# Optimization experiments

Hardware: AMD Instinct MI355X
Metric: run time of the kernel (lower is better)

Reference implementation:

```python
import jax, jax.numpy as jnp
import numpy as np

B, T, D = 2, 2048, 2048
H, KVH, HD = 32, 8, 64
N_REP = H // KVH


def setup_inputs() -> dict:
    key = jax.random.key(0)
    ks = jax.random.split(key, 7)
    x = jax.random.normal(ks[0], (B, T, D), dtype=jnp.float32)
    # rope tables: [max_seq, head_dim//2]
    cos = jax.random.uniform(ks[1], (T, HD // 2), dtype=jnp.float32, minval=-1.0, maxval=1.0)
    sin = jax.random.uniform(ks[2], (T, HD // 2), dtype=jnp.float32, minval=-1.0, maxval=1.0)
    s = 0.02
    wq = jax.random.normal(ks[3], (D, H * HD), dtype=jnp.float32) * s
    wk = jax.random.normal(ks[4], (D, KVH * HD), dtype=jnp.float32) * s
    wv = jax.random.normal(ks[5], (D, KVH * HD), dtype=jnp.float32) * s
    wo = jax.random.normal(ks[6], (H * HD, D), dtype=jnp.float32) * s
    return {"x": x, "cos": cos, "sin": sin, "wq": wq, "wk": wk, "wv": wv, "wo": wo}


def _rotate(t):
    h = t.shape[-1] // 2
    return jnp.concatenate([-t[..., h:], t[..., :h]], axis=-1)


def reference(x, cos, sin, wq, wk, wv, wo):
    b, t, _ = x.shape
    # projections -> [B, heads, T, HD]
    q = (x @ wq).reshape(b, t, H, HD).transpose(0, 2, 1, 3)
    k = (x @ wk).reshape(b, t, KVH, HD).transpose(0, 2, 1, 3)
    v = (x @ wv).reshape(b, t, KVH, HD).transpose(0, 2, 1, 3)
    # rope: cos/sin tiled (concat) to full head_dim, broadcast over batch/head
    cos_f = jnp.tile(cos[:t], (1, 2))[None, None]  # [1,1,T,HD]
    sin_f = jnp.tile(sin[:t], (1, 2))[None, None]
    q = q * cos_f + _rotate(q) * sin_f
    k = k * cos_f + _rotate(k) * sin_f
    # GQA: repeat kv heads
    k = jnp.repeat(k, N_REP, axis=1)
    v = jnp.repeat(v, N_REP, axis=1)
    scale = 1.0 / np.sqrt(HD).astype(np.float32)
    scores = jnp.einsum('bhqd,bhkd->bhqk', q, k) * scale
    causal = jnp.tril(jnp.ones((t, t), dtype=bool))
    scores = jnp.where(causal, scores, jnp.float32(-1e30))
    attn = jax.nn.softmax(scores, axis=-1)
    out = jnp.einsum('bhqk,bhkd->bhqd', attn, v)
    out = out.transpose(0, 2, 1, 3).reshape(b, t, H * HD)
    return out @ wo
```

## Files before the change

kernel.cpp:

```cpp
#include <hip/hip_runtime.h>
#include <hip/hip_bf16.h>
#include <cstdint>

typedef unsigned short u16;
typedef unsigned int u32;
typedef __bf16 bf16x8 __attribute__((ext_vector_type(8)));
typedef float f32x4 __attribute__((ext_vector_type(4)));
typedef float f32x16 __attribute__((ext_vector_type(16)));

#define BATCH 2
#define SEQ 2048
#define DMODEL 2048
#define NH 32
#define NKVH 8
#define HD 64
#define NQROWS (BATCH*SEQ)
#define QCOLS (NH*HD)
#define KVCOLS (NKVH*HD)
#define NCAT (QCOLS+2*KVCOLS)

static __device__ __forceinline__ u16 f2bf(float f) {
  u32 u = __float_as_uint(f);
  return (u16)((u + 0x7fffu + ((u >> 16) & 1u)) >> 16);
}

#define GLOAD16(gp, lp) __builtin_amdgcn_global_load_lds( \
    (const __attribute__((address_space(1))) void*)(gp),  \
    (__attribute__((address_space(3))) void*)(lp), 16, 0, 0)

__global__ __launch_bounds__(256) void k_cvt_bf16(const float* __restrict__ in,
                                                  u16* __restrict__ out, int n4) {
  int i = blockIdx.x * 256 + threadIdx.x;
  if (i >= n4) return;
  float4 v = reinterpret_cast<const float4*>(in)[i];
  ushort4 o;
  o.x = f2bf(v.x); o.y = f2bf(v.y); o.z = f2bf(v.z); o.w = f2bf(v.w);
  reinterpret_cast<ushort4*>(out)[i] = o;
}

__global__ __launch_bounds__(256) void k_transpose_all(const float* __restrict__ wq,
                                                       const float* __restrict__ wk,
                                                       const float* __restrict__ wv,
                                                       const float* __restrict__ wo,
                                                       u16* __restrict__ wcatT,
                                                       u16* __restrict__ woT) {
  __shared__ float tile[32][33];
  const int tidx = blockIdx.x;
  const float* src; u16* dst; int C, c0, r0;
  if (tidx < 4096) {
    src = wq; dst = wcatT; C = QCOLS;
    c0 = (tidx & 63) * 32; r0 = (tidx >> 6) * 32;
  } else if (tidx < 5120) {
    int t2 = tidx - 4096;
    src = wk; dst = wcatT + (size_t)QCOLS * DMODEL; C = KVCOLS;
    c0 = (t2 & 15) * 32; r0 = (t2 >> 4) * 32;
  } else if (tidx < 6144) {
    int t2 = tidx - 5120;
    src = wv; dst = wcatT + (size_t)(QCOLS + KVCOLS) * DMODEL; C = KVCOLS;
    c0 = (t2 & 15) * 32; r0 = (t2 >> 4) * 32;
  } else {
    int t2 = tidx - 6144;
    src = wo; dst = woT; C = DMODEL;
    c0 = (t2 & 63) * 32; r0 = (t2 >> 6) * 32;
  }
  const int R = 2048;
  int tx = threadIdx.x & 31, ty = threadIdx.x >> 5;
#pragma unroll
  for (int i = 0; i < 4; i++)
    tile[ty * 4 + i][tx] = src[(size_t)(r0 + ty * 4 + i) * C + c0 + tx];
  __syncthreads();
#pragma unroll
  for (int i = 0; i < 4; i++)
    dst[(size_t)(c0 + ty * 4 + i) * R + r0 + tx] = f2bf(tile[tx][ty * 4 + i]);
}

template<int EPI>
__global__ __launch_bounds__(256) void k_gemm(const u16* __restrict__ A,
                                              const u16* __restrict__ BT,
                                              void* __restrict__ Cout,
                                              int M, int N, int K,
                                              const float* __restrict__ cosb,
                                              const float* __restrict__ sinb,
                                              u16* __restrict__ dstK,
                                              u16* __restrict__ dstV) {
  __shared__ __align__(16) u16 As[2][128 * 32];
  __shared__ __align__(16) u16 Bs[2][128 * 32];
  const int tid = threadIdx.x;
  const int w = tid >> 6, l = tid & 63;
  const int l15 = l & 15, l4 = l >> 4;

  const int nwg = gridDim.x * gridDim.y;
  int hwid = blockIdx.y * gridDim.x + blockIdx.x;
  int wk = (hwid & 7) * (nwg >> 3) + (hwid >> 3);
  const int bx = wk % gridDim.x, by = wk / gridDim.x;

  const int m0 = by * 128, n0 = bx * 128;
  const int wr = w >> 1, wc = w & 1;

  const u16* ga = A + (size_t)(m0 + w * 32 + (l >> 2)) * K + (l & 3) * 8;
  const u16* gb = BT + (size_t)(n0 + w * 32 + (l >> 2)) * K + (l & 3) * 8;
  const int af_off = (wr * 64 + l15) * 32 + l4 * 8;
  const int bf_off = (wc * 64 + l15) * 32 + l4 * 8;

  auto stage = [&](int buf, int kt) {
    const u16* ga_ = ga + kt;
    const u16* gb_ = gb + kt;
    u16* asb = &As[buf][w * 1024];
    u16* bsb = &Bs[buf][w * 1024];
    GLOAD16(ga_, asb);
    GLOAD16(ga_ + 16 * (size_t)K, asb + 512);
    GLOAD16(gb_, bsb);
    GLOAD16(gb_ + 16 * (size_t)K, bsb + 512);
  };

  f32x4 acc[4][4] = {};
  stage(0, 0);
  __syncthreads();

  int cur = 0;
  for (int kt = 0; kt < K; kt += 32) {
    if (kt + 32 < K) stage(cur ^ 1, kt + 32);
    bf16x8 af[4], bfv[4];
#pragma unroll
    for (int mi = 0; mi < 4; mi++)
      af[mi] = *reinterpret_cast<const bf16x8*>(&As[cur][af_off + mi * 512]);
#pragma unroll
    for (int ni = 0; ni < 4; ni++)
      bfv[ni] = *reinterpret_cast<const bf16x8*>(&Bs[cur][bf_off + ni * 512]);
#pragma unroll
    for (int mi = 0; mi < 4; mi++)
#pragma unroll
      for (int ni = 0; ni < 4; ni++)
        acc[mi][ni] = __builtin_amdgcn_mfma_f32_16x16x32_bf16(af[mi], bfv[ni], acc[mi][ni], 0, 0, 0);
    __syncthreads();
    cur ^= 1;
  }

  const int row0 = m0 + wr * 64 + l4 * 4;
  const int col0 = n0 + wc * 64 + l15;
  if constexpr (EPI == 1) {
    float* C = (float*)Cout;
#pragma unroll
    for (int mi = 0; mi < 4; mi++)
#pragma unroll
      for (int ni = 0; ni < 4; ni++)
#pragma unroll
        for (int j = 0; j < 4; j++)
          C[(size_t)(row0 + mi * 16 + j) * N + col0 + ni * 16] = acc[mi][ni][j];
  } else {
    if (n0 < QCOLS + KVCOLS) {
#pragma unroll
      for (int mi = 0; mi < 4; mi++)
#pragma unroll
        for (int j = 0; j < 4; j++) {
          int t = (row0 + mi * 16 + j) & (SEQ - 1);
#pragma unroll
          for (int ni = 0; ni < 2; ni++) {
            int d = ni * 16 + l15;
            float c = cosb[t * 32 + d], s = sinb[t * 32 + d];
            float a = acc[mi][ni][j], bb = acc[mi][ni + 2][j];
            acc[mi][ni][j]     = a * c - bb * s;
            acc[mi][ni + 2][j] = bb * c + a * s;
          }
        }
      if (n0 < QCOLS) {
        const float QSC = 0.125f * 1.44269504088896f;
        u16* C = (u16*)Cout;
#pragma unroll
        for (int mi = 0; mi < 4; mi++)
#pragma unroll
          for (int ni = 0; ni < 4; ni++)
#pragma unroll
            for (int j = 0; j < 4; j++)
              C[(size_t)(row0 + mi * 16 + j) * QCOLS + col0 + ni * 16] = f2bf(acc[mi][ni][j] * QSC);
      } else {
        int kc0 = col0 - QCOLS;
#pragma unroll
        for (int mi = 0; mi < 4; mi++)
#pragma unroll
          for (int ni = 0; ni < 4; ni++)
#pragma unroll
            for (int j = 0; j < 4; j++)
              dstK[(size_t)(row0 + mi * 16 + j) * KVCOLS + kc0 + ni * 16] = f2bf(acc[mi][ni][j]);
      }
    } else {
      int vc0 = col0 - (QCOLS + KVCOLS);
#pragma unroll
      for (int mi = 0; mi < 4; mi++) {
        int row = row0 + mi * 16;
        int b = row >> 11, t = row & (SEQ - 1);
#pragma unroll
        for (int ni = 0; ni < 4; ni++) {
          ushort4 v;
          v.x = f2bf(acc[mi][ni][0]);
          v.y = f2bf(acc[mi][ni][1]);
          v.z = f2bf(acc[mi][ni][2]);
          v.w = f2bf(acc[mi][ni][3]);
          *reinterpret_cast<ushort4*>(&dstV[((size_t)b * KVCOLS + vc0 + ni * 16) * SEQ + t]) = v;
        }
      }
    }
  }
}

__global__ __launch_bounds__(128, 3) void k_attn(const u16* __restrict__ Q,
                                                 const u16* __restrict__ K,
                                                 const u16* __restrict__ VT,
                                                 u16* __restrict__ AO) {
  __shared__ __align__(16) u16 Ks[2][4096];
  __shared__ __align__(16) u16 Vs[2][4096];
  const int tid = threadIdx.x;
  const int w = tid >> 6, l = tid & 63;
  const int lo = l & 31, hi = l >> 5;
  const int id = blockIdx.y * gridDim.x + blockIdx.x;
  const int bh = (id & 7) * 8 + ((id >> 3) & 7);
  const int bxx = id >> 6;
  const int b = bh >> 5, h = bh & 31, g = h >> 2;
  const int srow = l >> 3;
  const int scol = l & 7;

  const u16* Kbase = K + ((size_t)b * SEQ) * KVCOLS + g * 64;
  const u16* Vbase = VT + ((size_t)(b * KVCOLS + g * 64)) * SEQ;

  for (int half = 0; half < 2; half++) {
    const int qt = half ? (31 - bxx) : bxx;
    const int qbase = qt * 64 + w * 32;
    const int nkc = qt + 1;
    const int qloc = w * 32 + lo;

    bf16x8 qf[4];
    {
      const u16* qp = Q + (size_t)(b * SEQ + qbase + lo) * QCOLS + h * 64 + hi * 8;
#pragma unroll
      for (int kb = 0; kb < 4; kb++)
        qf[kb] = *reinterpret_cast<const bf16x8*>(qp + kb * 16);
    }
    f32x16 oacc[2] = {};
    float ls0 = 0.f, ls1 = 0.f;

#pragma unroll
    for (int i = 0; i < 4; i++) {
      int r = w * 32 + i * 8 + srow;
      int cs = scol ^ (srow & 7);
      GLOAD16(Kbase + (size_t)r * KVCOLS + cs * 8, &Ks[0][(w * 32 + i * 8) * 64 + l * 8]);
      GLOAD16(Vbase + (size_t)r * SEQ + cs * 8, &Vs[0][(w * 32 + i * 8) * 64 + l * 8]);
    }
    __syncthreads();

    for (int kc = 0; kc < nkc; kc++) {
      const int bi = kc & 1;
      if (kc + 1 < nkc) {
#pragma unroll
        for (int i = 0; i < 4; i++) {
          int r = w * 32 + i * 8 + srow;
          int cs = scol ^ (srow & 7);
          GLOAD16(Kbase + (size_t)((kc + 1) * 64 + r) * KVCOLS + cs * 8,
                  &Ks[bi ^ 1][(w * 32 + i * 8) * 64 + l * 8]);
          GLOAD16(Vbase + (size_t)r * SEQ + (kc + 1) * 64 + cs * 8,
                  &Vs[bi ^ 1][(w * 32 + i * 8) * 64 + l * 8]);
        }
      }
      f32x16 sacc[2] = {};
      __builtin_amdgcn_s_setprio(1);
#pragma unroll
      for (int t = 0; t < 2; t++) {
#pragma unroll
        for (int kb = 0; kb < 4; kb++) {
          int row = t * 32 + lo;
          int slot = (2 * kb + hi) ^ (lo & 7);
          bf16x8 kf = *reinterpret_cast<const bf16x8*>(&Ks[bi][row * 64 + slot * 8]);
          sacc[t] = __builtin_amdgcn_mfma_f32_32x32x16_bf16(kf, qf[kb], sacc[t], 0, 0, 0);
        }
      }
      __builtin_amdgcn_s_setprio(0);

      const bool diag = (kc == qt);
      u32 u[2][4][2];
#pragma unroll
      for (int t = 0; t < 2; t++) {
        float pv[16];
#pragma unroll
        for (int r = 0; r < 16; r++) {
          float e = exp2f(sacc[t][r]);
          if (diag) {
            int kvoff = t * 32 + (r & 3) + 8 * (r >> 2) + 4 * hi;
            if (kvoff > qloc) e = 0.f;
          }
          pv[r] = e;
          if (t == 0) ls0 += e; else ls1 += e;
        }
#pragma unroll
        for (int qd = 0; qd < 4; qd++)
#pragma unroll
          for (int hh = 0; hh < 2; hh++) {
            u32 uu;
            asm("v_cvt_pk_bf16_f32 %0, %1, %2"
                : "=v"(uu) : "v"(pv[qd * 4 + 2 * hh]), "v"(pv[qd * 4 + 2 * hh + 1]));
            u[t][qd][hh] = uu;
          }
      }

#pragma unroll
      for (int km = 0; km < 4; km++) {
        const int t = km >> 1, p = km & 1;
        u32 a0 = u[t][2 * p][0], b0 = u[t][2 * p + 1][0];
        u32 a1 = u[t][2 * p][1], b1 = u[t][2 * p + 1][1];
        asm("v_permlane32_swap_b32 %0, %1" : "+v"(a0), "+v"(b0));
        asm("v_permlane32_swap_b32 %0, %1" : "+v"(a1), "+v"(b1));
        union { u32 uu[4]; bf16x8 v; } pa;
        pa.uu[0] = a0; pa.uu[1] = a1; pa.uu[2] = b0; pa.uu[3] = b1;
        __builtin_amdgcn_s_setprio(1);
#pragma unroll
        for (int td = 0; td < 2; td++) {
          int row = td * 32 + lo;
          int slot = (2 * km + hi) ^ (lo & 7);
          bf16x8 vf = *reinterpret_cast<const bf16x8*>(&Vs[bi][row * 64 + slot * 8]);
          oacc[td] = __builtin_amdgcn_mfma_f32_32x32x16_bf16(pa.v, vf, oacc[td], 0, 0, 0);
        }
        __builtin_amdgcn_s_setprio(0);
      }
      __syncthreads();
    }
    float tot = ls0 + ls1;
    tot += __shfl_xor(tot, 32);
#pragma unroll
    for (int r = 0; r < 16; r++) {
      int qr = (r & 3) + 8 * (r >> 2) + 4 * hi;
      float den = __shfl(tot, qr);
      float rv = __builtin_amdgcn_rcpf(den);
      size_t rowbase = (size_t)(b * SEQ + qbase + qr) * QCOLS + h * 64 + lo;
      AO[rowbase]      = f2bf(oacc[0][r] * rv);
      AO[rowbase + 32] = f2bf(oacc[1][r] * rv);
    }
  }
}

extern "C" void kernel_launch(void* const* d_in, const int* in_sizes, int n_in,
                              void* d_out, int out_size, void* d_ws, size_t ws_size,
                              hipStream_t stream) {
  const float* x    = (const float*)d_in[0];
  const float* cosb = (const float*)d_in[1];
  const float* sinb = (const float*)d_in[2];
  const float* wq   = (const float*)d_in[3];
  const float* wk   = (const float*)d_in[4];
  const float* wv   = (const float*)d_in[5];
  const float* wo   = (const float*)d_in[6];
  float* out = (float*)d_out;

  char* ws = (char*)d_ws;
  size_t off = 0;
  auto alloc = [&](size_t bytes) -> void* {
    void* p = ws + off;
    off += (bytes + 255) & ~(size_t)255;
    return p;
  };
  u16* xb    = (u16*)alloc((size_t)NQROWS * DMODEL * 2);
  u16* wcatT = (u16*)alloc((size_t)NCAT * DMODEL * 2);
  u16* woT   = (u16*)alloc((size_t)DMODEL * QCOLS * 2);
  u16* Qb    = (u16*)alloc((size_t)NQROWS * QCOLS * 2);
  u16* Kb    = (u16*)alloc((size_t)NQROWS * KVCOLS * 2);
  u16* VTb   = (u16*)alloc((size_t)BATCH * KVCOLS * SEQ * 2);
  u16* AO    = (u16*)alloc((size_t)NQROWS * QCOLS * 2);

  k_cvt_bf16<<<dim3(NQROWS * DMODEL / 4 / 256), dim3(256), 0, stream>>>(x, xb, NQROWS * DMODEL / 4);
  k_transpose_all<<<dim3(10240), dim3(256), 0, stream>>>(wq, wk, wv, wo, wcatT, woT);

  k_gemm<3><<<dim3(NCAT / 128, NQROWS / 128), 256, 0, stream>>>(
      xb, wcatT, Qb, NQROWS, NCAT, DMODEL, cosb, sinb, Kb, VTb);

  k_attn<<<dim3(16, BATCH * NH), 128, 0, stream>>>(Qb, Kb, VTb, AO);

  k_gemm<1><<<dim3(DMODEL / 128, NQROWS / 128), 256, 0, stream>>>(
      AO, woT, out, NQROWS, DMODEL, QCOLS, nullptr, nullptr, nullptr, nullptr);
}
```

Measured before the change: 214.5 us.

## Use single-wave attention blocks with 32-row tiles and waitcnt-based pipelining

```diff
diff --git a/kernel.cpp b/kernel.cpp
--- a/kernel.cpp
+++ b/kernel.cpp
@@ -203,108 +203,99 @@
   }
 }
 
-__global__ __launch_bounds__(128, 3) void k_attn(const u16* __restrict__ Q,
-                                                 const u16* __restrict__ K,
-                                                 const u16* __restrict__ VT,
-                                                 u16* __restrict__ AO) {
-  __shared__ __align__(16) u16 Ks[2][4096];
-  __shared__ __align__(16) u16 Vs[2][4096];
-  const int tid = threadIdx.x;
-  const int w = tid >> 6, l = tid & 63;
+__global__ __launch_bounds__(64, 3) void k_attn(const u16* __restrict__ Q,
+                                                const u16* __restrict__ K,
+                                                const u16* __restrict__ VT,
+                                                u16* __restrict__ AO) {
+  __shared__ __align__(16) u16 Ks[2][2048];
+  __shared__ __align__(16) u16 Vs[2][2048];
+  const int l = threadIdx.x;
   const int lo = l & 31, hi = l >> 5;
   const int id = blockIdx.y * gridDim.x + blockIdx.x;
   const int bh = (id & 7) * 8 + ((id >> 3) & 7);
   const int bxx = id >> 6;
   const int b = bh >> 5, h = bh & 31, g = h >> 2;
-  const int srow = l >> 3;
-  const int scol = l & 7;
 
   const u16* Kbase = K + ((size_t)b * SEQ) * KVCOLS + g * 64;
   const u16* Vbase = VT + ((size_t)(b * KVCOLS + g * 64)) * SEQ;
 
+  const int ksrow = l >> 3, kscol = l & 7;
+  const int kcs = kscol ^ ksrow;
+  const int vsrow = l >> 2, vscol = l & 3;
+  const int vcs = vscol ^ (vsrow & 3);
+
+  auto stage = [&](int kc, int buf) {
+#pragma unroll
+    for (int i = 0; i < 4; i++) {
+      GLOAD16(Kbase + (size_t)(kc * 32 + i * 8 + ksrow) * KVCOLS + kcs * 8,
+              &Ks[buf][i * 512 + l * 8]);
+      GLOAD16(Vbase + (size_t)(i * 16 + vsrow) * SEQ + kc * 32 + vcs * 8,
+              &Vs[buf][i * 512 + l * 8]);
+    }
+  };
+
   for (int half = 0; half < 2; half++) {
-    const int qt = half ? (31 - bxx) : bxx;
-    const int qbase = qt * 64 + w * 32;
+    const int qt = half ? (63 - bxx) : bxx;
+    const int q0 = qt * 32;
     const int nkc = qt + 1;
-    const int qloc = w * 32 + lo;
 
     bf16x8 qf[4];
     {
-      const u16* qp = Q + (size_t)(b * SEQ + qbase + lo) * QCOLS + h * 64 + hi * 8;
+      const u16* qp = Q + (size_t)(b * SEQ + q0 + lo) * QCOLS + h * 64 + hi * 8;
 #pragma unroll
       for (int kb = 0; kb < 4; kb++)
         qf[kb] = *reinterpret_cast<const bf16x8*>(qp + kb * 16);
     }
     f32x16 oacc[2] = {};
-    float ls0 = 0.f, ls1 = 0.f;
-
-#pragma unroll
-    for (int i = 0; i < 4; i++) {
-      int r = w * 32 + i * 8 + srow;
-      int cs = scol ^ (srow & 7);
-      GLOAD16(Kbase + (size_t)r * KVCOLS + cs * 8, &Ks[0][(w * 32 + i * 8) * 64 + l * 8]);
-      GLOAD16(Vbase + (size_t)r * SEQ + cs * 8, &Vs[0][(w * 32 + i * 8) * 64 + l * 8]);
-    }
-    __syncthreads();
-
+    float ls = 0.f;
+
+    stage(0, 0);
+    int bi = 0;
     for (int kc = 0; kc < nkc; kc++) {
-      const int bi = kc & 1;
       if (kc + 1 < nkc) {
-#pragma unroll
-        for (int i = 0; i < 4; i++) {
-          int r = w * 32 + i * 8 + srow;
-          int cs = scol ^ (srow & 7);
-          GLOAD16(Kbase + (size_t)((kc + 1) * 64 + r) * KVCOLS + cs * 8,
-                  &Ks[bi ^ 1][(w * 32 + i * 8) * 64 + l * 8]);
-          GLOAD16(Vbase + (size_t)r * SEQ + (kc + 1) * 64 + cs * 8,
-                  &Vs[bi ^ 1][(w * 32 + i * 8) * 64 + l * 8]);
-        }
-      }
-      f32x16 sacc[2] = {};
+        stage(kc + 1, bi ^ 1);
+        asm volatile("s_waitcnt vmcnt(8)" ::: "memory");
+      } else {
+        asm volatile("s_waitcnt vmcnt(0)" ::: "memory");
+      }
+      __builtin_amdgcn_sched_barrier(0);
+
+      f32x16 sacc = {};
       __builtin_amdgcn_s_setprio(1);
 #pragma unroll
-      for (int t = 0; t < 2; t++) {
-#pragma unroll
-        for (int kb = 0; kb < 4; kb++) {
-          int row = t * 32 + lo;
-          int slot = (2 * kb + hi) ^ (lo & 7);
-          bf16x8 kf = *reinterpret_cast<const bf16x8*>(&Ks[bi][row * 64 + slot * 8]);
-          sacc[t] = __builtin_amdgcn_mfma_f32_32x32x16_bf16(kf, qf[kb], sacc[t], 0, 0, 0);
-        }
+      for (int kb = 0; kb < 4; kb++) {
+        int slot = (2 * kb + hi) ^ (lo & 7);
+        bf16x8 kf = *reinterpret_cast<const bf16x8*>(&Ks[bi][lo * 64 + slot * 8]);
+        sacc = __builtin_amdgcn_mfma_f32_32x32x16_bf16(kf, qf[kb], sacc, 0, 0, 0);
       }
       __builtin_amdgcn_s_setprio(0);
 
       const bool diag = (kc == qt);
-      u32 u[2][4][2];
-#pragma unroll
-      for (int t = 0; t < 2; t++) {
-        float pv[16];
-#pragma unroll
-        for (int r = 0; r < 16; r++) {
-          float e = exp2f(sacc[t][r]);
-          if (diag) {
-            int kvoff = t * 32 + (r & 3) + 8 * (r >> 2) + 4 * hi;
-            if (kvoff > qloc) e = 0.f;
-          }
-          pv[r] = e;
-          if (t == 0) ls0 += e; else ls1 += e;
-        }
-#pragma unroll
-        for (int qd = 0; qd < 4; qd++)
-#pragma unroll
-          for (int hh = 0; hh < 2; hh++) {
-            u32 uu;
-            asm("v_cvt_pk_bf16_f32 %0, %1, %2"
-                : "=v"(uu) : "v"(pv[qd * 4 + 2 * hh]), "v"(pv[qd * 4 + 2 * hh + 1]));
-            u[t][qd][hh] = uu;
-          }
-      }
-
-#pragma unroll
-      for (int km = 0; km < 4; km++) {
-        const int t = km >> 1, p = km & 1;
-        u32 a0 = u[t][2 * p][0], b0 = u[t][2 * p + 1][0];
-        u32 a1 = u[t][2 * p][1], b1 = u[t][2 * p + 1][1];
+      float pv[16];
+#pragma unroll
+      for (int r = 0; r < 16; r++) {
+        float e = exp2f(sacc[r]);
+        if (diag) {
+          int kvg = kc * 32 + (r & 3) + 8 * (r >> 2) + 4 * hi;
+          if (kvg > q0 + lo) e = 0.f;
+        }
+        pv[r] = e; ls += e;
+      }
+      u32 u[4][2];
+#pragma unroll
+      for (int qd = 0; qd < 4; qd++)
+#pragma unroll
+        for (int hh = 0; hh < 2; hh++) {
+          u32 uu;
+          asm("v_cvt_pk_bf16_f32 %0, %1, %2"
+              : "=v"(uu) : "v"(pv[qd * 4 + 2 * hh]), "v"(pv[qd * 4 + 2 * hh + 1]));
+          u[qd][hh] = uu;
+        }
+
+#pragma unroll
+      for (int km = 0; km < 2; km++) {
+        u32 a0 = u[2 * km][0], b0 = u[2 * km + 1][0];
+        u32 a1 = u[2 * km][1], b1 = u[2 * km + 1][1];
         asm("v_permlane32_swap_b32 %0, %1" : "+v"(a0), "+v"(b0));
         asm("v_permlane32_swap_b32 %0, %1" : "+v"(a1), "+v"(b1));
         union { u32 uu[4]; bf16x8 v; } pa;
@@ -313,22 +304,22 @@
 #pragma unroll
         for (int td = 0; td < 2; td++) {
           int row = td * 32 + lo;
-          int slot = (2 * km + hi) ^ (lo & 7);
-          bf16x8 vf = *reinterpret_cast<const bf16x8*>(&Vs[bi][row * 64 + slot * 8]);
+          int slot = (2 * km + hi) ^ (lo & 3);
+          bf16x8 vf = *reinterpret_cast<const bf16x8*>(&Vs[bi][row * 32 + slot * 8]);
           oacc[td] = __builtin_amdgcn_mfma_f32_32x32x16_bf16(pa.v, vf, oacc[td], 0, 0, 0);
         }
         __builtin_amdgcn_s_setprio(0);
       }
-      __syncthreads();
-    }
-    float tot = ls0 + ls1;
+      bi ^= 1;
+    }
+    float tot = ls;
     tot += __shfl_xor(tot, 32);
 #pragma unroll
     for (int r = 0; r < 16; r++) {
       int qr = (r & 3) + 8 * (r >> 2) + 4 * hi;
       float den = __shfl(tot, qr);
       float rv = __builtin_amdgcn_rcpf(den);
-      size_t rowbase = (size_t)(b * SEQ + qbase + qr) * QCOLS + h * 64 + lo;
+      size_t rowbase = (size_t)(b * SEQ + q0 + qr) * QCOLS + h * 64 + lo;
       AO[rowbase]      = f2bf(oacc[0][r] * rv);
       AO[rowbase + 32] = f2bf(oacc[1][r] * rv);
     }
@@ -368,7 +359,7 @@
   k_gemm<3><<<dim3(NCAT / 128, NQROWS / 128), 256, 0, stream>>>(
       xb, wcatT, Qb, NQROWS, NCAT, DMODEL, cosb, sinb, Kb, VTb);
 
-  k_attn<<<dim3(16, BATCH * NH), 128, 0, stream>>>(Qb, Kb, VTb, AO);
+  k_attn<<<dim3(32, BATCH * NH), 64, 0, stream>>>(Qb, Kb, VTb, AO);
 
   k_gemm<1><<<dim3(DMODEL / 128, NQROWS / 128), 256, 0, stream>>>(
       AO, woT, out, NQROWS, DMODEL, QCOLS, nullptr, nullptr, nullptr, nullptr);
```

Result: slower. 229.0 us (+6.7%).

## Process both causal query tiles in one KV sweep sharing staged K/V

Applied to the files above, without the earlier changes.

```diff
diff --git a/kernel.cpp b/kernel.cpp
--- a/kernel.cpp
+++ b/kernel.cpp
@@ -203,7 +203,7 @@
   }
 }
 
-__global__ __launch_bounds__(128, 3) void k_attn(const u16* __restrict__ Q,
+__global__ __launch_bounds__(128, 2) void k_attn(const u16* __restrict__ Q,
                                                  const u16* __restrict__ K,
                                                  const u16* __restrict__ VT,
                                                  u16* __restrict__ AO) {
@@ -216,78 +216,81 @@
   const int bh = (id & 7) * 8 + ((id >> 3) & 7);
   const int bxx = id >> 6;
   const int b = bh >> 5, h = bh & 31, g = h >> 2;
-  const int srow = l >> 3;
-  const int scol = l & 7;
+  const int srow = l >> 3, scol = l & 7;
 
   const u16* Kbase = K + ((size_t)b * SEQ) * KVCOLS + g * 64;
   const u16* Vbase = VT + ((size_t)(b * KVCOLS + g * 64)) * SEQ;
 
-  for (int half = 0; half < 2; half++) {
-    const int qt = half ? (31 - bxx) : bxx;
-    const int qbase = qt * 64 + w * 32;
-    const int nkc = qt + 1;
-    const int qloc = w * 32 + lo;
-
-    bf16x8 qf[4];
-    {
-      const u16* qp = Q + (size_t)(b * SEQ + qbase + lo) * QCOLS + h * 64 + hi * 8;
-#pragma unroll
-      for (int kb = 0; kb < 4; kb++)
-        qf[kb] = *reinterpret_cast<const bf16x8*>(qp + kb * 16);
-    }
-    f32x16 oacc[2] = {};
-    float ls0 = 0.f, ls1 = 0.f;
-
-#pragma unroll
-    for (int i = 0; i < 4; i++) {
-      int r = w * 32 + i * 8 + srow;
-      int cs = scol ^ (srow & 7);
-      GLOAD16(Kbase + (size_t)r * KVCOLS + cs * 8, &Ks[0][(w * 32 + i * 8) * 64 + l * 8]);
-      GLOAD16(Vbase + (size_t)r * SEQ + cs * 8, &Vs[0][(w * 32 + i * 8) * 64 + l * 8]);
-    }
-    __syncthreads();
-
-    for (int kc = 0; kc < nkc; kc++) {
-      const int bi = kc & 1;
-      if (kc + 1 < nkc) {
-#pragma unroll
-        for (int i = 0; i < 4; i++) {
-          int r = w * 32 + i * 8 + srow;
-          int cs = scol ^ (srow & 7);
-          GLOAD16(Kbase + (size_t)((kc + 1) * 64 + r) * KVCOLS + cs * 8,
-                  &Ks[bi ^ 1][(w * 32 + i * 8) * 64 + l * 8]);
-          GLOAD16(Vbase + (size_t)r * SEQ + (kc + 1) * 64 + cs * 8,
-                  &Vs[bi ^ 1][(w * 32 + i * 8) * 64 + l * 8]);
-        }
-      }
-      f32x16 sacc[2] = {};
+  const int qtA = bxx;
+  const int qtB = 31 - bxx;
+  const int q0A = qtA * 64 + w * 32;
+  const int q0B = qtB * 64 + w * 32;
+  const int nkc = qtB + 1;
+  const int qloc = w * 32 + lo;
+
+  bf16x8 qfA[4], qfB[4];
+  {
+    const u16* qpA = Q + (size_t)(b * SEQ + q0A + lo) * QCOLS + h * 64 + hi * 8;
+    const u16* qpB = Q + (size_t)(b * SEQ + q0B + lo) * QCOLS + h * 64 + hi * 8;
+#pragma unroll
+    for (int kb = 0; kb < 4; kb++) {
+      qfA[kb] = *reinterpret_cast<const bf16x8*>(qpA + kb * 16);
+      qfB[kb] = *reinterpret_cast<const bf16x8*>(qpB + kb * 16);
+    }
+  }
+  f32x16 oaccA[2] = {}, oaccB[2] = {};
+  float lsA = 0.f, lsB = 0.f;
+
+#pragma unroll
+  for (int i = 0; i < 4; i++) {
+    int r = w * 32 + i * 8 + srow;
+    int cs = scol ^ (srow & 7);
+    GLOAD16(Kbase + (size_t)r * KVCOLS + cs * 8, &Ks[0][(w * 32 + i * 8) * 64 + l * 8]);
+    GLOAD16(Vbase + (size_t)r * SEQ + cs * 8, &Vs[0][(w * 32 + i * 8) * 64 + l * 8]);
+  }
+  __syncthreads();
+
+  for (int kc = 0; kc < nkc; kc++) {
+    const int bi = kc & 1;
+    if (kc + 1 < nkc) {
+#pragma unroll
+      for (int i = 0; i < 4; i++) {
+        int r = w * 32 + i * 8 + srow;
+        int cs = scol ^ (srow & 7);
+        GLOAD16(Kbase + (size_t)((kc + 1) * 64 + r) * KVCOLS + cs * 8,
+                &Ks[bi ^ 1][(w * 32 + i * 8) * 64 + l * 8]);
+        GLOAD16(Vbase + (size_t)r * SEQ + (kc + 1) * 64 + cs * 8,
+                &Vs[bi ^ 1][(w * 32 + i * 8) * 64 + l * 8]);
+      }
+    }
+    const bool doA = (kc <= qtA);
+    u32 uA[2][4][2], uB[2][4][2];
+
+    if (doA) {
+      f32x16 saccA[2] = {};
       __builtin_amdgcn_s_setprio(1);
 #pragma unroll
-      for (int t = 0; t < 2; t++) {
+      for (int t = 0; t < 2; t++)
 #pragma unroll
         for (int kb = 0; kb < 4; kb++) {
           int row = t * 32 + lo;
           int slot = (2 * kb + hi) ^ (lo & 7);
           bf16x8 kf = *reinterpret_cast<const bf16x8*>(&Ks[bi][row * 64 + slot * 8]);
-          sacc[t] = __builtin_amdgcn_mfma_f32_32x32x16_bf16(kf, qf[kb], sacc[t], 0, 0, 0);
-        }
-      }
+          saccA[t] = __builtin_amdgcn_mfma_f32_32x32x16_bf16(kf, qfA[kb], saccA[t], 0, 0, 0);
+        }
       __builtin_amdgcn_s_setprio(0);
-
-      const bool diag = (kc == qt);
-      u32 u[2][4][2];
+      const bool diagA = (kc == qtA);
 #pragma unroll
       for (int t = 0; t < 2; t++) {
         float pv[16];
 #pragma unroll
         for (int r = 0; r < 16; r++) {
-          float e = exp2f(sacc[t][r]);
-          if (diag) {
+          float e = exp2f(saccA[t][r]);
+          if (diagA) {
             int kvoff = t * 32 + (r & 3) + 8 * (r >> 2) + 4 * hi;
             if (kvoff > qloc) e = 0.f;
           }
-          pv[r] = e;
-          if (t == 0) ls0 += e; else ls1 += e;
+          pv[r] = e; lsA += e;
         }
 #pragma unroll
         for (int qd = 0; qd < 4; qd++)
@@ -296,15 +299,55 @@
             u32 uu;
             asm("v_cvt_pk_bf16_f32 %0, %1, %2"
                 : "=v"(uu) : "v"(pv[qd * 4 + 2 * hh]), "v"(pv[qd * 4 + 2 * hh + 1]));
-            u[t][qd][hh] = uu;
+            uA[t][qd][hh] = uu;
           }
       }
-
+    }
+
+    {
+      f32x16 saccB[2] = {};
+      __builtin_amdgcn_s_setprio(1);
+#pragma unroll
+      for (int t = 0; t < 2; t++)
+#pragma unroll
+        for (int kb = 0; kb < 4; kb++) {
+          int row = t * 32 + lo;
+          int slot = (2 * kb + hi) ^ (lo & 7);
+          bf16x8 kf = *reinterpret_cast<const bf16x8*>(&Ks[bi][row * 64 + slot * 8]);
+          saccB[t] = __builtin_amdgcn_mfma_f32_32x32x16_bf16(kf, qfB[kb], saccB[t], 0, 0, 0);
+        }
+      __builtin_amdgcn_s_setprio(0);
+      const bool diagB = (kc == qtB);
+#pragma unroll
+      for (int t = 0; t < 2; t++) {
+        float pv[16];
+#pragma unroll
+        for (int r = 0; r < 16; r++) {
+          float e = exp2f(saccB[t][r]);
+          if (diagB) {
+            int kvoff = t * 32 + (r & 3) + 8 * (r >> 2) + 4 * hi;
+            if (kvoff > qloc) e = 0.f;
+          }
+          pv[r] = e; lsB += e;
+        }
+#pragma unroll
+        for (int qd = 0; qd < 4; qd++)
+#pragma unroll
+          for (int hh = 0; hh < 2; hh++) {
+            u32 uu;
+            asm("v_cvt_pk_bf16_f32 %0, %1, %2"
+                : "=v"(uu) : "v"(pv[qd * 4 + 2 * hh]), "v"(pv[qd * 4 + 2 * hh + 1]));
+            uB[t][qd][hh] = uu;
+          }
+      }
+    }
+
+    if (doA) {
 #pragma unroll
       for (int km = 0; km < 4; km++) {
         const int t = km >> 1, p = km & 1;
-        u32 a0 = u[t][2 * p][0], b0 = u[t][2 * p + 1][0];
-        u32 a1 = u[t][2 * p][1], b1 = u[t][2 * p + 1][1];
+        u32 a0 = uA[t][2 * p][0], b0 = uA[t][2 * p + 1][0];
+        u32 a1 = uA[t][2 * p][1], b1 = uA[t][2 * p + 1][1];
         asm("v_permlane32_swap_b32 %0, %1" : "+v"(a0), "+v"(b0));
         asm("v_permlane32_swap_b32 %0, %1" : "+v"(a1), "+v"(b1));
         union { u32 uu[4]; bf16x8 v; } pa;
@@ -315,22 +358,57 @@
           int row = td * 32 + lo;
           int slot = (2 * km + hi) ^ (lo & 7);
           bf16x8 vf = *reinterpret_cast<const bf16x8*>(&Vs[bi][row * 64 + slot * 8]);
-          oacc[td] = __builtin_amdgcn_mfma_f32_32x32x16_bf16(pa.v, vf, oacc[td], 0, 0, 0);
+          oaccA[td] = __builtin_amdgcn_mfma_f32_32x32x16_bf16(pa.v, vf, oaccA[td], 0, 0, 0);
         }
         __builtin_amdgcn_s_setprio(0);
       }
-      __syncthreads();
-    }
-    float tot = ls0 + ls1;
+    }
+#pragma unroll
+    for (int km = 0; km < 4; km++) {
+      const int t = km >> 1, p = km & 1;
+      u32 a0 = uB[t][2 * p][0], b0 = uB[t][2 * p + 1][0];
+      u32 a1 = uB[t][2 * p][1], b1 = uB[t][2 * p + 1][1];
+      asm("v_permlane32_swap_b32 %0, %1" : "+v"(a0), "+v"(b0));
+      asm("v_permlane32_swap_b32 %0, %1" : "+v"(a1), "+v"(b1));
+      union { u32 uu[4]; bf16x8 v; } pa;
+      pa.uu[0] = a0; pa.uu[1] = a1; pa.uu[2] = b0; pa.uu[3] = b1;
+      __builtin_amdgcn_s_setprio(1);
+#pragma unroll
+      for (int td = 0; td < 2; td++) {
+        int row = td * 32 + lo;
+        int slot = (2 * km + hi) ^ (lo & 7);
+        bf16x8 vf = *reinterpret_cast<const bf16x8*>(&Vs[bi][row * 64 + slot * 8]);
+        oaccB[td] = __builtin_amdgcn_mfma_f32_32x32x16_bf16(pa.v, vf, oaccB[td], 0, 0, 0);
+      }
+      __builtin_amdgcn_s_setprio(0);
+    }
+    __syncthreads();
+  }
+
+  {
+    float tot = lsA;
     tot += __shfl_xor(tot, 32);
 #pragma unroll
     for (int r = 0; r < 16; r++) {
       int qr = (r & 3) + 8 * (r >> 2) + 4 * hi;
       float den = __shfl(tot, qr);
       float rv = __builtin_amdgcn_rcpf(den);
-      size_t rowbase = (size_t)(b * SEQ + qbase + qr) * QCOLS + h * 64 + lo;
-      AO[rowbase]      = f2bf(oacc[0][r] * rv);
-      AO[rowbase + 32] = f2bf(oacc[1][r] * rv);
+      size_t rowbase = (size_t)(b * SEQ + q0A + qr) * QCOLS + h * 64 + lo;
+      AO[rowbase]      = f2bf(oaccA[0][r] * rv);
+      AO[rowbase + 32] = f2bf(oaccA[1][r] * rv);
+    }
+  }
+  {
+    float tot = lsB;
+    tot += __shfl_xor(tot, 32);
+#pragma unroll
+    for (int r = 0; r < 16; r++) {
+      int qr = (r & 3) + 8 * (r >> 2) + 4 * hi;
+      float den = __shfl(tot, qr);
+      float rv = __builtin_amdgcn_rcpf(den);
+      size_t rowbase = (size_t)(b * SEQ + q0B + qr) * QCOLS + h * 64 + lo;
+      AO[rowbase]      = f2bf(oaccB[0][r] * rv);
+      AO[rowbase + 32] = f2bf(oaccB[1][r] * rv);
     }
   }
 }
```

New measurement: 202.7 us. 5.5% less time.
